# Kernel tuning notes

Hardware: AMD Instinct MI355X
Metric: run time of the kernel (lower is better)

## Reference

```python
import jax, jax.numpy as jnp
import numpy as np


def _wn(W, g):
    # weight_norm with dim=None: scalar g times W / ||W||_F
    return (g / jnp.linalg.norm(W)) * W


def setup_inputs() -> dict:
    key = jax.random.key(0)
    ks = jax.random.split(key, 8)
    B, N, D = 16, 1024, 128
    v_dim = q_dim = 1024
    K = 1024 * 3  # h_dim * k
    h_out = 8
    s = 0.02
    return {
        "v": jax.random.normal(ks[0], (B, N, v_dim), jnp.float32),
        "q": jax.random.normal(ks[1], (B, D, q_dim), jnp.float32),
        "Wv": jax.random.normal(ks[2], (K, v_dim), jnp.float32) * s,
        "gv": jnp.ones((), jnp.float32),
        "bv": jax.random.normal(ks[3], (K,), jnp.float32) * s,
        "Wq": jax.random.normal(ks[4], (K, q_dim), jnp.float32) * s,
        "gq": jnp.ones((), jnp.float32),
        "bq": jax.random.normal(ks[5], (K,), jnp.float32) * s,
        "h_mat": jax.random.normal(ks[6], (1, h_out, 1, K), jnp.float32) * s,
        "h_bias": jnp.zeros((1, h_out, 1, 1), jnp.float32),
    }


def reference(v, q, Wv, gv, bv, Wq, gq, bq, h_mat, h_bias):
    # v_net / q_net: single weight-normed Linear (dropout inactive at inference)
    v_ = jnp.einsum('bnc,kc->bnk', v, _wn(Wv, gv)) + bv  # (B,N,K)
    q_ = jnp.einsum('bdc,kc->bdk', q, _wn(Wq, gq)) + bq  # (B,D,K)
    hm = h_mat[0, :, 0, :]                               # (H,K)
    # logits[b,h,n,d] = sum_k hm[h,k] * v_[b,n,k] * q_[b,d,k]
    logits = jnp.einsum('hk,bnk,bdk->bhnd', hm, v_, q_) + h_bias
    return logits
```

## Files before the change

### kernel.cpp

```cpp
#include <hip/hip_runtime.h>
#include <hip/hip_bf16.h>
#include <math.h>

typedef unsigned short u16;
typedef unsigned int u32;

typedef __bf16 bf16x8 __attribute__((ext_vector_type(8)));
typedef float f32x4 __attribute__((ext_vector_type(4)));

union U8 { uint4 u; u16 s[8]; };

__device__ __forceinline__ float b2f(u16 x) {
    u32 y = ((u32)x) << 16;
    return __builtin_bit_cast(float, y);
}
__device__ __forceinline__ u16 f2b(float f) {
    u32 x = __builtin_bit_cast(u32, f);
    u32 r = x + 0x7fffu + ((x >> 16) & 1u);
    return (u16)(r >> 16);
}
__device__ __forceinline__ uint4 cvt8(float4 a, float4 b) {
    U8 o;
    o.s[0] = f2b(a.x); o.s[1] = f2b(a.y); o.s[2] = f2b(a.z); o.s[3] = f2b(a.w);
    o.s[4] = f2b(b.x); o.s[5] = f2b(b.y); o.s[6] = f2b(b.z); o.s[7] = f2b(b.w);
    return o.u;
}

__device__ __forceinline__ void gload16(const u16* g, const u16* l) {
    __builtin_amdgcn_global_load_lds(
        (const __attribute__((address_space(1))) void*)g,
        (__attribute__((address_space(3))) void*)l, 16, 0, 0);
}


__global__ void __launch_bounds__(64) zero_ss(float* ss) {
    if (threadIdx.x < 2) ss[threadIdx.x] = 0.f;
}

__global__ void __launch_bounds__(256) sumsq_k(const float* __restrict__ Wv,
                                               const float* __restrict__ Wq,
                                               float* __restrict__ ss, int n) {
    const float* W = (blockIdx.y == 0) ? Wv : Wq;
    float acc = 0.f;
    size_t stride = (size_t)gridDim.x * 256 * 8;
    for (size_t i = ((size_t)blockIdx.x * 256 + threadIdx.x) * 8; i < (size_t)n; i += stride) {
        float4 a = *(const float4*)(W + i);
        float4 b = *(const float4*)(W + i + 4);
        acc += a.x * a.x + a.y * a.y + a.z * a.z + a.w * a.w;
        acc += b.x * b.x + b.y * b.y + b.z * b.z + b.w * b.w;
    }
#pragma unroll
    for (int o = 32; o > 0; o >>= 1) acc += __shfl_down(acc, o, 64);
    __shared__ float red[4];
    int lane = threadIdx.x & 63, wv = threadIdx.x >> 6;
    if (lane == 0) red[wv] = acc;
    __syncthreads();
    if (threadIdx.x == 0) atomicAdd(&ss[blockIdx.y], red[0] + red[1] + red[2] + red[3]);
}

__global__ void __launch_bounds__(256) twvh_k(const float* __restrict__ Wv,
                                              const float* __restrict__ hm,
                                              u16* __restrict__ wvh) {
    __shared__ float t[32][33];
    int cx0 = blockIdx.x * 32;
    int ky0 = blockIdx.y * 32;
    int tx = threadIdx.x, ty = threadIdx.y;
#pragma unroll
    for (int j = ty; j < 32; j += 8)
        t[j][tx] = Wv[(size_t)(ky0 + j) * 1024 + cx0 + tx];
    __syncthreads();
    int k = ky0 + tx;
    float hv[8];
#pragma unroll
    for (int h = 0; h < 8; h++) hv[h] = hm[(size_t)h * 3072 + k];
#pragma unroll
    for (int j = ty; j < 32; j += 8) {
        float w = t[tx][j];
        int c = cx0 + j;
#pragma unroll
        for (int h = 0; h < 8; h++)
            wvh[(size_t)h * 3145728 + (size_t)c * 3072 + k] = f2b(hv[h] * w);
    }
}

__global__ void __launch_bounds__(256) cvt_v(const float* __restrict__ v,
                                             u16* __restrict__ vb, int n) {
    size_t stride = (size_t)gridDim.x * 256 * 8;
    for (size_t i = ((size_t)blockIdx.x * 256 + threadIdx.x) * 8; i < (size_t)n; i += stride) {
        float4 a = *(const float4*)(v + i);
        float4 b = *(const float4*)(v + i + 4);
        *(uint4*)(vb + i) = cvt8(a, b);
    }
}

__global__ void __launch_bounds__(256) const_k(const u16* __restrict__ qbuf,
                                               const float* __restrict__ bv,
                                               const float* __restrict__ hm,
                                               float* __restrict__ cb) {
    int idx = blockIdx.x * 256 + threadIdx.x;
    int b = idx >> 10, hd = idx & 1023, h = hd >> 7, d = hd & 127;
    const u16* qr = qbuf + ((size_t)b * 128 + d) * 3072;
    const float* hr = hm + (size_t)h * 3072;
    float acc = 0.f;
    for (int k = 0; k < 3072; k += 8) {
        U8 uq; uq.u = *(const uint4*)(qr + k);
        float4 h0 = *(const float4*)(hr + k);
        float4 h1 = *(const float4*)(hr + k + 4);
        float4 b0 = *(const float4*)(bv + k);
        float4 b1 = *(const float4*)(bv + k + 4);
        acc += b2f(uq.s[0]) * h0.x * b0.x + b2f(uq.s[1]) * h0.y * b0.y +
               b2f(uq.s[2]) * h0.z * b0.z + b2f(uq.s[3]) * h0.w * b0.w +
               b2f(uq.s[4]) * h1.x * b1.x + b2f(uq.s[5]) * h1.y * b1.y +
               b2f(uq.s[6]) * h1.z * b1.z + b2f(uq.s[7]) * h1.w * b1.w;
    }
    cb[idx] = acc;
}

template <int EPI, bool A_BF16>
__global__ void __launch_bounds__(256)
gemm_bt(const void* __restrict__ Ap, const u16* __restrict__ Bp, void* __restrict__ C,
        const float* __restrict__ ss, int ss_idx, const float* __restrict__ g,
        const float* __restrict__ bias, const float* __restrict__ cb,
        const float* __restrict__ hbias, int kdim, size_t abatch, size_t bbatch) {
    constexpr int BK = 32;
    __shared__ __align__(16) u16 sA[2][128 * BK];
    __shared__ __align__(16) u16 sB[2][128 * BK];

    const int tid = threadIdx.x;
    const int lane = tid & 63, wv = tid >> 6;
    const int wm = (wv & 1) * 64, wn = (wv >> 1) * 64;
    const int lr = lane & 15, quad = lane >> 4;
    const int z = blockIdx.z;
    const int arow0 = blockIdx.y * 128;
    const int bcol0 = blockIdx.x * 128;

    const size_t aoff = (size_t)z * abatch;
    const size_t boff = (size_t)z * bbatch;

    const int srow = 16 * wv + (lane >> 2);
    const int qcg  = (lane & 3) ^ ((lane >> 3) & 3);
    const int lb0  = wv * 512;
    const int lb1  = lb0 + 2048;

    const u16* gB0 = Bp + boff + (size_t)(bcol0 + srow) * kdim + qcg * 8;
    const u16* gB1 = gB0 + (size_t)64 * kdim;

    const int r0 = tid >> 2, c0 = (tid & 3) * 8;
    const int w0 = r0 * 32 + (((tid & 3) ^ ((tid >> 3) & 3)) * 8);
    const int w1 = w0 + 2048;

    const u16* gA0 = nullptr; const u16* gA1 = nullptr;
    const float* fA0 = nullptr; const float* fA1 = nullptr;
    if constexpr (A_BF16) {
        gA0 = (const u16*)Ap + aoff + (size_t)(arow0 + srow) * kdim + qcg * 8;
        gA1 = gA0 + (size_t)64 * kdim;
    } else {
        fA0 = (const float*)Ap + aoff + (size_t)(arow0 + r0) * kdim + c0;
        fA1 = fA0 + (size_t)64 * kdim;
    }

    const int rsw = (quad ^ ((lr >> 1) & 3)) * 8;

    if constexpr (A_BF16) {
        gload16(gA0, sA[0] + lb0);
        gload16(gA1, sA[0] + lb1);
        gA0 += BK; gA1 += BK;
    } else {
        float4 x0 = *(const float4*)fA0, x1 = *(const float4*)(fA0 + 4);
        float4 y0 = *(const float4*)fA1, y1 = *(const float4*)(fA1 + 4);
        *(uint4*)(sA[0] + w0) = cvt8(x0, x1);
        *(uint4*)(sA[0] + w1) = cvt8(y0, y1);
        fA0 += BK; fA1 += BK;
    }
    gload16(gB0, sB[0] + lb0);
    gload16(gB1, sB[0] + lb1);
    gB0 += BK; gB1 += BK;

    f32x4 acc[4][4];
#pragma unroll
    for (int im = 0; im < 4; im++)
#pragma unroll
        for (int in = 0; in < 4; in++) acc[im][in] = (f32x4){0.f, 0.f, 0.f, 0.f};

    __syncthreads();

    int p = 0;
    for (int kt = 0; kt < kdim; kt += BK) {
        const bool more = (kt + BK < kdim);

        float4 ax0, ax1, ay0, ay1;
        if (more) {
            if constexpr (A_BF16) {
                gload16(gA0, sA[p ^ 1] + lb0);
                gload16(gA1, sA[p ^ 1] + lb1);
                gA0 += BK; gA1 += BK;
            } else {
                ax0 = *(const float4*)fA0; ax1 = *(const float4*)(fA0 + 4);
                ay0 = *(const float4*)fA1; ay1 = *(const float4*)(fA1 + 4);
                fA0 += BK; fA1 += BK;
            }
            gload16(gB0, sB[p ^ 1] + lb0);
            gload16(gB1, sB[p ^ 1] + lb1);
            gB0 += BK; gB1 += BK;
        }

        const u16* sAp = sA[p];
        const u16* sBp = sB[p];
        bf16x8 af[4], bfr[4];
#pragma unroll
        for (int im = 0; im < 4; im++)
            af[im] = *(const bf16x8*)(sAp + (wm + im * 16 + lr) * 32 + rsw);
#pragma unroll
        for (int in = 0; in < 4; in++)
            bfr[in] = *(const bf16x8*)(sBp + (wn + in * 16 + lr) * 32 + rsw);
#pragma unroll
        for (int im = 0; im < 4; im++)
#pragma unroll
            for (int in = 0; in < 4; in++)
                acc[im][in] = __builtin_amdgcn_mfma_f32_16x16x32_bf16(af[im], bfr[in], acc[im][in], 0, 0, 0);

        if (more) {
            if constexpr (!A_BF16) {
                u16* dA = sA[p ^ 1];
                *(uint4*)(dA + w0) = cvt8(ax0, ax1);
                *(uint4*)(dA + w1) = cvt8(ay0, ay1);
            }
        }
        __syncthreads();
        p ^= 1;
    }

    float scale = 1.f;
    if constexpr (EPI == 0 || EPI == 2) scale = g[0] / sqrtf(ss[ss_idx]);

#pragma unroll
    for (int im = 0; im < 4; im++) {
#pragma unroll
        for (int in = 0; in < 4; in++) {
#pragma unroll
            for (int reg = 0; reg < 4; reg++) {
                int gr = arow0 + wm + im * 16 + quad * 4 + reg;
                int gc = bcol0 + wn + in * 16 + lr;
                float val = acc[im][in][reg];
                if constexpr (EPI == 0) {
                    ((u16*)C)[(size_t)gr * 3072 + gc] = f2b(val * scale + bias[gc]);
                } else if constexpr (EPI == 1) {
                    size_t idx = (((size_t)(gr >> 7) * 8 + (gc >> 10)) * 128 + (gr & 127)) * 1024
                               + (gc & 1023);
                    ((u16*)C)[idx] = f2b(val);
                } else {
                    int h = gc >> 7, d = gc & 127;
                    float o = val * scale + cb[(size_t)z * 1024 + gc] + hbias[h];
                    ((float*)C)[(((size_t)z * 8 + h) * 1024 + gr) * 128 + d] = o;
                }
            }
        }
    }
}

template <int EPI>
__global__ void __launch_bounds__(512, 2)
gemm8p(const u16* __restrict__ Ap, const u16* __restrict__ Bp, void* __restrict__ C,
       const float* __restrict__ ss, const float* __restrict__ g,
       const float* __restrict__ cb, const float* __restrict__ hbias,
       int kdim, size_t abatch, size_t bbatch) {
    __shared__ __align__(16) u16 sA[2][256 * 64];
    __shared__ __align__(16) u16 sB[2][256 * 64];

    const int tid = threadIdx.x;
    const int lane = tid & 63, wv = tid >> 6;
    const int wm = (wv & 1) * 128;
    const int wn = (wv >> 1) * 64;
    const int lr = lane & 15, quad = lane >> 4;
    const int z = blockIdx.z;

    int bx, by;
    if constexpr (EPI == 1) {
        int orig = blockIdx.y * 32 + blockIdx.x;
        int xcd = orig & 7, idx = orig >> 3;
        bx = (xcd << 2) | (idx & 3);
        by = idx >> 2;
    } else {
        bx = blockIdx.x; by = blockIdx.y;
    }
    const int arow0 = by * 256, bcol0 = bx * 256;

    const size_t aoff = (size_t)z * abatch, boff = (size_t)z * bbatch;

    const int sg = (tid & 7) ^ ((tid >> 3) & 7);
    const u16* gA = Ap + aoff + (size_t)(arow0 + (tid >> 3)) * kdim + sg * 8;
    const u16* gB = Bp + boff + (size_t)(bcol0 + (tid >> 3)) * kdim + sg * 8;
    const size_t ldk64 = (size_t)64 * kdim;
    const int ldst = wv * 512;

    const int slot = (quad ^ (lane & 7)) * 8;
    const int rbA = (wm + lr) * 64 + slot;
    const int rbB = (wn + lr) * 64 + slot;

    f32x4 acc[8][4];
#pragma unroll
    for (int im = 0; im < 8; im++)
#pragma unroll
        for (int in = 0; in < 4; in++) acc[im][in] = (f32x4){0.f, 0.f, 0.f, 0.f};

    gload16(gA + 0 * ldk64, sA[0] + 0 * 4096 + ldst);
    gload16(gA + 1 * ldk64, sA[0] + 1 * 4096 + ldst);
    gload16(gA + 2 * ldk64, sA[0] + 2 * 4096 + ldst);
    gload16(gA + 3 * ldk64, sA[0] + 3 * 4096 + ldst);
    gload16(gB + 0 * ldk64, sB[0] + 0 * 4096 + ldst);
    gload16(gB + 1 * ldk64, sB[0] + 1 * 4096 + ldst);
    gload16(gB + 2 * ldk64, sB[0] + 2 * 4096 + ldst);
    gload16(gB + 3 * ldk64, sB[0] + 3 * 4096 + ldst);
    gA += 64; gB += 64;
    asm volatile("s_waitcnt vmcnt(0)" ::: "memory");
    __builtin_amdgcn_s_barrier();

    const int NT = kdim >> 6;
    bf16x8 af[4], bfr[4];
    for (int t = 0; t < NT; ++t) {
        const u16* sAd = sA[t & 1];
        const u16* sBd = sB[t & 1];
        u16* dA = sA[(t & 1) ^ 1];
        u16* dB = sB[(t & 1) ^ 1];
        const bool stg = (t + 1 < NT);

#pragma unroll
        for (int n = 0; n < 4; n++) bfr[n] = *(const bf16x8*)(sBd + rbB + n * 1024);
#pragma unroll
        for (int j = 0; j < 4; j++) af[j] = *(const bf16x8*)(sAd + rbA + j * 1024);
        if (stg) {
            gload16(gA + 0 * ldk64, dA + 0 * 4096 + ldst);
            gload16(gA + 2 * ldk64, dA + 2 * 4096 + ldst);
        }
        __builtin_amdgcn_s_barrier();
        __builtin_amdgcn_s_setprio(1);
#pragma unroll
        for (int j = 0; j < 4; j++)
#pragma unroll
            for (int n = 0; n < 4; n++)
                acc[j][n] = __builtin_amdgcn_mfma_f32_16x16x32_bf16(af[j], bfr[n], acc[j][n], 0, 0, 0);
        __builtin_amdgcn_s_setprio(0);
        if (stg) asm volatile("s_waitcnt vmcnt(2)" ::: "memory");
        else     asm volatile("s_waitcnt vmcnt(0)" ::: "memory");
        __builtin_amdgcn_s_barrier();

#pragma unroll
        for (int j = 0; j < 4; j++) af[j] = *(const bf16x8*)(sAd + rbA + (4 + j) * 1024);
        if (stg) {
            gload16(gB + 0 * ldk64, dB + 0 * 4096 + ldst);
            gload16(gB + 1 * ldk64, dB + 1 * 4096 + ldst);
        }
        __builtin_amdgcn_s_barrier();
        __builtin_amdgcn_s_setprio(1);
#pragma unroll
        for (int j = 0; j < 4; j++)
#pragma unroll
            for (int n = 0; n < 4; n++)
                acc[4 + j][n] = __builtin_amdgcn_mfma_f32_16x16x32_bf16(af[j], bfr[n], acc[4 + j][n], 0, 0, 0);
        __builtin_amdgcn_s_setprio(0);
        __builtin_amdgcn_s_barrier();

#pragma unroll
        for (int n = 0; n < 4; n++) bfr[n] = *(const bf16x8*)(sBd + (rbB ^ 32) + n * 1024);
#pragma unroll
        for (int j = 0; j < 4; j++) af[j] = *(const bf16x8*)(sAd + (rbA ^ 32) + j * 1024);
        if (stg) {
            gload16(gB + 2 * ldk64, dB + 2 * 4096 + ldst);
            gload16(gB + 3 * ldk64, dB + 3 * 4096 + ldst);
        }
        __builtin_amdgcn_s_barrier();
        __builtin_amdgcn_s_setprio(1);
#pragma unroll
        for (int j = 0; j < 4; j++)
#pragma unroll
            for (int n = 0; n < 4; n++)
                acc[j][n] = __builtin_amdgcn_mfma_f32_16x16x32_bf16(af[j], bfr[n], acc[j][n], 0, 0, 0);
        __builtin_amdgcn_s_setprio(0);
        __builtin_amdgcn_s_barrier();

#pragma unroll
        for (int j = 0; j < 4; j++) af[j] = *(const bf16x8*)(sAd + (rbA ^ 32) + (4 + j) * 1024);
        if (stg) {
            gload16(gA + 1 * ldk64, dA + 1 * 4096 + ldst);
            gload16(gA + 3 * ldk64, dA + 3 * 4096 + ldst);
        }
        __builtin_amdgcn_s_barrier();
        __builtin_amdgcn_s_setprio(1);
#pragma unroll
        for (int j = 0; j < 4; j++)
#pragma unroll
            for (int n = 0; n < 4; n++)
                acc[4 + j][n] = __builtin_amdgcn_mfma_f32_16x16x32_bf16(af[j], bfr[n], acc[4 + j][n], 0, 0, 0);
        __builtin_amdgcn_s_setprio(0);
        if (stg) asm volatile("s_waitcnt vmcnt(2)" ::: "memory");
        __builtin_amdgcn_s_barrier();

        gA += 64; gB += 64;
    }

    float scale = 1.f;
    if constexpr (EPI == 2) scale = g[0] / sqrtf(ss[0]);

#pragma unroll
    for (int im = 0; im < 8; im++) {
#pragma unroll
        for (int in = 0; in < 4; in++) {
#pragma unroll
            for (int reg = 0; reg < 4; reg++) {
                int gr = arow0 + wm + im * 16 + quad * 4 + reg;
                int gc = bcol0 + wn + in * 16 + lr;
                float val = acc[im][in][reg];
                if constexpr (EPI == 1) {
                    size_t idx = (((size_t)(gr >> 7) * 8 + (gc >> 10)) * 128 + (gr & 127)) * 1024
                               + (gc & 1023);
                    ((u16*)C)[idx] = f2b(val);
                } else {
                    int h = gc >> 7, d = gc & 127;
                    float o = val * scale + cb[(size_t)z * 1024 + gc] + hbias[h];
                    ((float*)C)[(((size_t)z * 8 + h) * 1024 + gr) * 128 + d] = o;
                }
            }
        }
    }
}


extern "C" void kernel_launch(void* const* d_in, const int* in_sizes, int n_in,
                              void* d_out, int out_size, void* d_ws, size_t ws_size,
                              hipStream_t stream) {
    (void)in_sizes; (void)n_in; (void)out_size;
    const float* v  = (const float*)d_in[0];
    const float* q  = (const float*)d_in[1];
    const float* Wv = (const float*)d_in[2];
    const float* gv = (const float*)d_in[3];
    const float* bv = (const float*)d_in[4];
    const float* Wq = (const float*)d_in[5];
    const float* gq = (const float*)d_in[6];
    const float* bq = (const float*)d_in[7];
    const float* hm = (const float*)d_in[8];
    const float* hb = (const float*)d_in[9];
    float* out = (float*)d_out;

    char* ws = (char*)d_ws;
    float* ss   = (float*)ws;
    float* cb   = (float*)(ws + 256);
    u16*   qbuf = (u16*)(ws + 256 + 65536);
    u16*   tbuf = (u16*)(ws + 256 + 65536 + 12582912);
    u16*   vb   = (u16*)(ws + 256 + 65536 + 12582912 + 33554432);
    const size_t need_vb = 256 + 65536 + 12582912 + 33554432 + 33554432;
    const bool fullfat = (ws_size >= need_vb);

    u16* wvh = (u16*)d_out;
    u16* qb  = (u16*)((char*)d_out + 50331648);
    u16* wqb = (u16*)((char*)d_out + 54525952);

    zero_ss<<<1, 64, 0, stream>>>(ss);
    sumsq_k<<<dim3(256, 2), 256, 0, stream>>>(Wv, Wq, ss, 3072 * 1024);

    twvh_k<<<dim3(32, 96), dim3(32, 8), 0, stream>>>(Wv, hm, wvh);

    cvt_v<<<1024, 256, 0, stream>>>(q, qb, 2097152);
    cvt_v<<<1536, 256, 0, stream>>>(Wq, wqb, 3145728);

    gemm_bt<0, true><<<dim3(24, 16, 1), 256, 0, stream>>>(
        qb, wqb, qbuf, ss, 1, gq, bq, nullptr, nullptr, 1024, 0, 0);

    const_k<<<64, 256, 0, stream>>>(qbuf, bv, hm, cb);

    gemm8p<1><<<dim3(32, 8, 1), 512, 0, stream>>>(
        qbuf, wvh, tbuf, nullptr, nullptr, nullptr, nullptr, 3072, 0, 0);

    if (fullfat) {
        cvt_v<<<4096, 256, 0, stream>>>(v, vb, 16777216);
        gemm8p<2><<<dim3(4, 4, 16), 512, 0, stream>>>(
            vb, tbuf, out, ss, gv, cb, hb, 1024, 1048576, 1048576);
    } else {
        gemm_bt<2, false><<<dim3(8, 8, 16), 256, 0, stream>>>(
            v, tbuf, out, ss, 0, gv, nullptr, cb, hb, 1024, 1048576, 1048576);
    }
}
```

Measured before the change: 402.4 us.

## Double-buffer MFMA fragments in registers and prefetch the next tile early

```diff
diff --git a/kernel.cpp b/kernel.cpp
--- a/kernel.cpp
+++ b/kernel.cpp
@@ -264,8 +264,8 @@
        const float* __restrict__ ss, const float* __restrict__ g,
        const float* __restrict__ cb, const float* __restrict__ hbias,
        int kdim, size_t abatch, size_t bbatch) {
-    __shared__ __align__(16) u16 sA[2][256 * 64];
-    __shared__ __align__(16) u16 sB[2][256 * 64];
+    __shared__ __align__(16) u16 sAb[2][256 * 64];
+    __shared__ __align__(16) u16 sBb[2][256 * 64];
 
     const int tid = threadIdx.x;
     const int lane = tid & 63, wv = tid >> 6;
@@ -303,84 +303,58 @@
 #pragma unroll
         for (int in = 0; in < 4; in++) acc[im][in] = (f32x4){0.f, 0.f, 0.f, 0.f};
 
-    gload16(gA + 0 * ldk64, sA[0] + 0 * 4096 + ldst);
-    gload16(gA + 1 * ldk64, sA[0] + 1 * 4096 + ldst);
-    gload16(gA + 2 * ldk64, sA[0] + 2 * 4096 + ldst);
-    gload16(gA + 3 * ldk64, sA[0] + 3 * 4096 + ldst);
-    gload16(gB + 0 * ldk64, sB[0] + 0 * 4096 + ldst);
-    gload16(gB + 1 * ldk64, sB[0] + 1 * 4096 + ldst);
-    gload16(gB + 2 * ldk64, sB[0] + 2 * 4096 + ldst);
-    gload16(gB + 3 * ldk64, sB[0] + 3 * 4096 + ldst);
+    const u16* sAd = sAb[0];
+    const u16* sBd = sBb[0];
+    u16* dA = (u16*)sAb[1];
+    u16* dB = (u16*)sBb[1];
+
+    gload16(gB + 0 * ldk64, sBb[0] + 0 * 4096 + ldst);
+    gload16(gB + 1 * ldk64, sBb[0] + 1 * 4096 + ldst);
+    gload16(gB + 2 * ldk64, sBb[0] + 2 * 4096 + ldst);
+    gload16(gB + 3 * ldk64, sBb[0] + 3 * 4096 + ldst);
+    gload16(gA + 0 * ldk64, sAb[0] + 0 * 4096 + ldst);
+    gload16(gA + 2 * ldk64, sAb[0] + 2 * 4096 + ldst);
+    gload16(gA + 1 * ldk64, sAb[0] + 1 * 4096 + ldst);
+    gload16(gA + 3 * ldk64, sAb[0] + 3 * 4096 + ldst);
     gA += 64; gB += 64;
     asm volatile("s_waitcnt vmcnt(0)" ::: "memory");
     __builtin_amdgcn_s_barrier();
 
+    bf16x8 af0[4], af1[4], bf0[4], bf1[4];
+#pragma unroll
+    for (int n = 0; n < 4; n++) bf0[n] = *(const bf16x8*)(sBd + rbB + n * 1024);
+#pragma unroll
+    for (int j = 0; j < 4; j++) af0[j] = *(const bf16x8*)(sAd + rbA + j * 1024);
+
     const int NT = kdim >> 6;
-    bf16x8 af[4], bfr[4];
     for (int t = 0; t < NT; ++t) {
-        const u16* sAd = sA[t & 1];
-        const u16* sBd = sB[t & 1];
-        u16* dA = sA[(t & 1) ^ 1];
-        u16* dB = sB[(t & 1) ^ 1];
         const bool stg = (t + 1 < NT);
 
 #pragma unroll
-        for (int n = 0; n < 4; n++) bfr[n] = *(const bf16x8*)(sBd + rbB + n * 1024);
-#pragma unroll
-        for (int j = 0; j < 4; j++) af[j] = *(const bf16x8*)(sAd + rbA + j * 1024);
+        for (int j = 0; j < 4; j++) af1[j] = *(const bf16x8*)(sAd + rbA + (4 + j) * 1024);
+        if (stg) {
+            gload16(gB + 0 * ldk64, dB + 0 * 4096 + ldst);
+            gload16(gB + 1 * ldk64, dB + 1 * 4096 + ldst);
+            gload16(gB + 2 * ldk64, dB + 2 * 4096 + ldst);
+            gload16(gB + 3 * ldk64, dB + 3 * 4096 + ldst);
+        }
+        __builtin_amdgcn_s_barrier();
+        __builtin_amdgcn_s_setprio(1);
+#pragma unroll
+        for (int j = 0; j < 4; j++)
+#pragma unroll
+            for (int n = 0; n < 4; n++)
+                acc[j][n] = __builtin_amdgcn_mfma_f32_16x16x32_bf16(af0[j], bf0[n], acc[j][n], 0, 0, 0);
+        __builtin_amdgcn_s_setprio(0);
+        __builtin_amdgcn_s_barrier();
+
+#pragma unroll
+        for (int n = 0; n < 4; n++) bf1[n] = *(const bf16x8*)(sBd + (rbB ^ 32) + n * 1024);
+#pragma unroll
+        for (int j = 0; j < 4; j++) af0[j] = *(const bf16x8*)(sAd + (rbA ^ 32) + j * 1024);
         if (stg) {
             gload16(gA + 0 * ldk64, dA + 0 * 4096 + ldst);
             gload16(gA + 2 * ldk64, dA + 2 * 4096 + ldst);
-        }
-        __builtin_amdgcn_s_barrier();
-        __builtin_amdgcn_s_setprio(1);
-#pragma unroll
-        for (int j = 0; j < 4; j++)
-#pragma unroll
-            for (int n = 0; n < 4; n++)
-                acc[j][n] = __builtin_amdgcn_mfma_f32_16x16x32_bf16(af[j], bfr[n], acc[j][n], 0, 0, 0);
-        __builtin_amdgcn_s_setprio(0);
-        if (stg) asm volatile("s_waitcnt vmcnt(2)" ::: "memory");
-        else     asm volatile("s_waitcnt vmcnt(0)" ::: "memory");
-        __builtin_amdgcn_s_barrier();
-
-#pragma unroll
-        for (int j = 0; j < 4; j++) af[j] = *(const bf16x8*)(sAd + rbA + (4 + j) * 1024);
-        if (stg) {
-            gload16(gB + 0 * ldk64, dB + 0 * 4096 + ldst);
-            gload16(gB + 1 * ldk64, dB + 1 * 4096 + ldst);
-        }
-        __builtin_amdgcn_s_barrier();
-        __builtin_amdgcn_s_setprio(1);
-#pragma unroll
-        for (int j = 0; j < 4; j++)
-#pragma unroll
-            for (int n = 0; n < 4; n++)
-                acc[4 + j][n] = __builtin_amdgcn_mfma_f32_16x16x32_bf16(af[j], bfr[n], acc[4 + j][n], 0, 0, 0);
-        __builtin_amdgcn_s_setprio(0);
-        __builtin_amdgcn_s_barrier();
-
-#pragma unroll
-        for (int n = 0; n < 4; n++) bfr[n] = *(const bf16x8*)(sBd + (rbB ^ 32) + n * 1024);
-#pragma unroll
-        for (int j = 0; j < 4; j++) af[j] = *(const bf16x8*)(sAd + (rbA ^ 32) + j * 1024);
-        if (stg) {
-            gload16(gB + 2 * ldk64, dB + 2 * 4096 + ldst);
-            gload16(gB + 3 * ldk64, dB + 3 * 4096 + ldst);
-        }
-        __builtin_amdgcn_s_barrier();
-        __builtin_amdgcn_s_setprio(1);
-#pragma unroll
-        for (int j = 0; j < 4; j++)
-#pragma unroll
-            for (int n = 0; n < 4; n++)
-                acc[j][n] = __builtin_amdgcn_mfma_f32_16x16x32_bf16(af[j], bfr[n], acc[j][n], 0, 0, 0);
-        __builtin_amdgcn_s_setprio(0);
-        __builtin_amdgcn_s_barrier();
-
-#pragma unroll
-        for (int j = 0; j < 4; j++) af[j] = *(const bf16x8*)(sAd + (rbA ^ 32) + (4 + j) * 1024);
-        if (stg) {
             gload16(gA + 1 * ldk64, dA + 1 * 4096 + ldst);
             gload16(gA + 3 * ldk64, dA + 3 * 4096 + ldst);
         }
@@ -390,11 +364,42 @@
         for (int j = 0; j < 4; j++)
 #pragma unroll
             for (int n = 0; n < 4; n++)
-                acc[4 + j][n] = __builtin_amdgcn_mfma_f32_16x16x32_bf16(af[j], bfr[n], acc[4 + j][n], 0, 0, 0);
+                acc[4 + j][n] = __builtin_amdgcn_mfma_f32_16x16x32_bf16(af1[j], bf0[n], acc[4 + j][n], 0, 0, 0);
         __builtin_amdgcn_s_setprio(0);
-        if (stg) asm volatile("s_waitcnt vmcnt(2)" ::: "memory");
-        __builtin_amdgcn_s_barrier();
-
+        __builtin_amdgcn_s_barrier();
+
+#pragma unroll
+        for (int j = 0; j < 4; j++) af1[j] = *(const bf16x8*)(sAd + (rbA ^ 32) + (4 + j) * 1024);
+        __builtin_amdgcn_s_barrier();
+        __builtin_amdgcn_s_setprio(1);
+#pragma unroll
+        for (int j = 0; j < 4; j++)
+#pragma unroll
+            for (int n = 0; n < 4; n++)
+                acc[j][n] = __builtin_amdgcn_mfma_f32_16x16x32_bf16(af0[j], bf1[n], acc[j][n], 0, 0, 0);
+        __builtin_amdgcn_s_setprio(0);
+        asm volatile("s_waitcnt vmcnt(2)" ::: "memory");
+        __builtin_amdgcn_s_barrier();
+
+        if (stg) {
+#pragma unroll
+            for (int n = 0; n < 4; n++) bf0[n] = *(const bf16x8*)(dB + rbB + n * 1024);
+#pragma unroll
+            for (int j = 0; j < 4; j++) af0[j] = *(const bf16x8*)(dA + rbA + j * 1024);
+        }
+        __builtin_amdgcn_s_barrier();
+        __builtin_amdgcn_s_setprio(1);
+#pragma unroll
+        for (int j = 0; j < 4; j++)
+#pragma unroll
+            for (int n = 0; n < 4; n++)
+                acc[4 + j][n] = __builtin_amdgcn_mfma_f32_16x16x32_bf16(af1[j], bf1[n], acc[4 + j][n], 0, 0, 0);
+        __builtin_amdgcn_s_setprio(0);
+        asm volatile("s_waitcnt vmcnt(0)" ::: "memory");
+        __builtin_amdgcn_s_barrier();
+
+        const u16* tp = sAd; sAd = dA; dA = (u16*)tp;
+        tp = sBd; sBd = dB; dB = (u16*)tp;
         gA += 64; gB += 64;
     }
 
```

Measured after the change: 403.8 us. No clear change (+0.3%).
